# Kernel optimization log

Measured on AMD Instinct MI355X. Metric: run time of the kernel, lower is better.

The kernel has to match this reference:

```python
import jax, jax.numpy as jnp
import numpy as np

EMBED_DIM = 1024
K_DIM = 64
NUM_HEADS = 16


def setup_inputs() -> dict:
    key = jax.random.key(0)
    kx, kq, kk, kv, kw = jax.random.split(key, 5)
    x = jax.random.normal(kx, (4, 2048, EMBED_DIM), dtype=jnp.float32)
    # per-head weights stacked along a leading head axis (torch.randn init)
    wq = jax.random.normal(kq, (NUM_HEADS, EMBED_DIM, K_DIM), dtype=jnp.float32)
    wk = jax.random.normal(kk, (NUM_HEADS, EMBED_DIM, K_DIM), dtype=jnp.float32)
    wv = jax.random.normal(kv, (NUM_HEADS, EMBED_DIM, K_DIM), dtype=jnp.float32)
    w = jax.random.normal(kw, (NUM_HEADS * K_DIM, EMBED_DIM), dtype=jnp.float32)
    return {"x": x, "wq": wq, "wk": wk, "wv": wv, "w": w}


def reference(x, wq, wk, wv, w):
    # x: [B,S,D]; wq/wk/wv: [H,D,K]; w: [H*K, D]
    q = jnp.einsum('bsd,hdk->bhsk', x, wq)
    k = jnp.einsum('bsd,hdk->bhsk', x, wk)
    v = jnp.einsum('bsd,hdk->bhsk', x, wv)
    scale = 1.0 / jnp.sqrt(jnp.asarray(K_DIM, x.dtype))
    scores = jnp.einsum('bhsk,bhtk->bhst', q, k) * scale  # [B,H,S,S]
    attn = jax.nn.softmax(scores, axis=-1)
    ctx = jnp.einsum('bhst,bhtk->bhsk', attn, v)  # [B,H,S,K]
    B, H, S, K = ctx.shape
    # concat heads along last dim in head order (matches torch.cat of per-head outs)
    heads = jnp.transpose(ctx, (0, 2, 1, 3)).reshape(B, S, H * K)
    return jnp.matmul(heads, w)  # [B,S,D]
```

## Files before the change

kernel.cpp:

```cpp
#include <hip/hip_runtime.h>
#include <hip/hip_bf16.h>
#include <math.h>

#define EMBED 1024
#define KD 64
#define NH 16
#define SEQ 2048
#define BATCH 4
#define BH (BATCH * NH)
#define NTOK ((size_t)BH * SEQ * KD)

typedef float4 f4;
typedef unsigned short u16;
typedef __attribute__((ext_vector_type(8))) short v8s;
typedef __attribute__((ext_vector_type(4))) float v4f;

__device__ __forceinline__ u16 f2bf(float f) {
    unsigned u = __float_as_uint(f);
    unsigned r = (u + 0x7fffu + ((u >> 16) & 1u)) >> 16;
    return (u16)r;
}
__device__ __forceinline__ float bf2f(u16 h) {
    return __uint_as_float(((unsigned)h) << 16);
}

__device__ __forceinline__ void gload_lds16(const void* g, void* l) {
    __builtin_amdgcn_global_load_lds(
        (const __attribute__((address_space(1))) unsigned int*)g,
        (__attribute__((address_space(3))) unsigned int*)l, 16, 0, 0);
}

__global__ __launch_bounds__(256)
void convert_all_kernel(const float* __restrict__ x,
                        const float* __restrict__ wq, const float* __restrict__ wk,
                        const float* __restrict__ wv, const float* __restrict__ w,
                        u16* __restrict__ xh, u16* __restrict__ xl,
                        u16* __restrict__ Wth, u16* __restrict__ Wtl,
                        u16* __restrict__ OWth, u16* __restrict__ OWtl)
{
    int b = blockIdx.x;
    if (b < 8192) {
        size_t i = ((size_t)b * 256 + threadIdx.x) * 4;
        f4 v = *(const f4*)(x + i);
        u16 h0 = f2bf(v.x), h1 = f2bf(v.y), h2 = f2bf(v.z), h3 = f2bf(v.w);
        u16 l0 = f2bf(v.x - bf2f(h0)), l1 = f2bf(v.y - bf2f(h1));
        u16 l2 = f2bf(v.z - bf2f(h2)), l3 = f2bf(v.w - bf2f(h3));
        uint2 H, L;
        H.x = (unsigned)h0 | ((unsigned)h1 << 16);
        H.y = (unsigned)h2 | ((unsigned)h3 << 16);
        L.x = (unsigned)l0 | ((unsigned)l1 << 16);
        L.y = (unsigned)l2 | ((unsigned)l3 << 16);
        *(uint2*)(xh + i) = H;
        *(uint2*)(xl + i) = L;
    } else if (b < 8192 + 3072) {
        int n = b - 8192;
        int mat = n >> 10, nin = n & 1023, h = nin >> 6, c = nin & 63;
        const float* __restrict__ ws = (mat == 0) ? wq : (mat == 1) ? wk : wv;
        float sc = (mat == 0) ? (0.125f * 1.4426950408889634f) : 1.0f;
        for (int d = threadIdx.x; d < EMBED; d += 256) {
            float f = ws[((size_t)h * EMBED + d) * KD + c] * sc;
            u16 hi = f2bf(f);
            u16 lo = f2bf(f - bf2f(hi));
            Wth[(size_t)n * EMBED + d] = hi;
            Wtl[(size_t)n * EMBED + d] = lo;
        }
    } else {
        int n = b - 11264;
        for (int k = threadIdx.x; k < EMBED; k += 256) {
            float f = w[(size_t)k * EMBED + n];
            u16 hi = f2bf(f);
            u16 lo = f2bf(f - bf2f(hi));
            OWth[(size_t)n * EMBED + k] = hi;
            OWtl[(size_t)n * EMBED + k] = lo;
        }
    }
}

__global__ __launch_bounds__(256)
void qkv_mfma_kernel(const u16* __restrict__ xh, const u16* __restrict__ xl,
                     const u16* __restrict__ Wth, const u16* __restrict__ Wtl,
                     u16* __restrict__ Qhi, u16* __restrict__ Qlo,
                     u16* __restrict__ Khi, u16* __restrict__ Klo,
                     u16* __restrict__ Vt)
{
    __shared__ u16 sAh[128 * 64];
    __shared__ u16 sAl[128 * 64];
    __shared__ u16 sBh[128 * 64];
    __shared__ u16 sBl[128 * 64];
    const int tid = threadIdx.x;
    const int lane = tid & 63, wid = tid >> 6;
    const int lm = lane & 15, lq = lane >> 4;
    const int wm = wid & 1, wn = wid >> 1;
    const int bid = blockIdx.y * 24 + blockIdx.x;
    const int swz = (bid & 7) * 192 + (bid >> 3);
    const int m0 = (swz / 24) * 128;
    const int n0 = (swz % 24) * 128;
    const bool three = (n0 < 2048);

    v4f acc[4][4];
#pragma unroll
    for (int mt = 0; mt < 4; ++mt)
#pragma unroll
        for (int nt = 0; nt < 4; ++nt)
            acc[mt][nt] = (v4f){0.f, 0.f, 0.f, 0.f};

    const int srow = wid * 32 + (lane >> 3);
    const int sblk = (lane & 7) ^ (lane >> 3);

    for (int k0 = 0; k0 < EMBED; k0 += 64) {
        __syncthreads();
#pragma unroll
        for (int i = 0; i < 4; ++i) {
            int row = srow + i * 8;
            size_t gA = (((size_t)(m0 + row)) << 10) + k0 + sblk * 8;
            size_t gB = (((size_t)(n0 + row)) << 10) + k0 + sblk * 8;
            int lo = (wid * 32 + i * 8) * 128;
            gload_lds16((const char*)xh + gA * 2, (char*)sAh + lo);
            gload_lds16((const char*)Wth + gB * 2, (char*)sBh + lo);
            if (three) {
                gload_lds16((const char*)xl + gA * 2, (char*)sAl + lo);
                gload_lds16((const char*)Wtl + gB * 2, (char*)sBl + lo);
            }
        }
        asm volatile("s_waitcnt vmcnt(0)" ::: "memory");
        __syncthreads();

#pragma unroll
        for (int kks = 0; kks < 2; ++kks) {
            v8s ah[4], bh[4];
            const int ba = ((kks * 4 + lq) ^ (lm & 7)) * 8;
#pragma unroll
            for (int t = 0; t < 4; ++t) {
                int ra = wm * 64 + t * 16 + lm;
                int rb = wn * 64 + t * 16 + lm;
                ah[t] = *(const v8s*)&sAh[ra * 64 + ba];
                bh[t] = *(const v8s*)&sBh[rb * 64 + ba];
            }
            if (three) {
                v8s al[4], bl[4];
#pragma unroll
                for (int t = 0; t < 4; ++t) {
                    int ra = wm * 64 + t * 16 + lm;
                    int rb = wn * 64 + t * 16 + lm;
                    al[t] = *(const v8s*)&sAl[ra * 64 + ba];
                    bl[t] = *(const v8s*)&sBl[rb * 64 + ba];
                }
#pragma unroll
                for (int mt = 0; mt < 4; ++mt)
#pragma unroll
                    for (int nt = 0; nt < 4; ++nt) {
                        acc[mt][nt] = __builtin_amdgcn_mfma_f32_16x16x32_bf16(ah[mt], bh[nt], acc[mt][nt], 0, 0, 0);
                        acc[mt][nt] = __builtin_amdgcn_mfma_f32_16x16x32_bf16(ah[mt], bl[nt], acc[mt][nt], 0, 0, 0);
                        acc[mt][nt] = __builtin_amdgcn_mfma_f32_16x16x32_bf16(al[mt], bh[nt], acc[mt][nt], 0, 0, 0);
                    }
            } else {
#pragma unroll
                for (int mt = 0; mt < 4; ++mt)
#pragma unroll
                    for (int nt = 0; nt < 4; ++nt)
                        acc[mt][nt] = __builtin_amdgcn_mfma_f32_16x16x32_bf16(ah[mt], bh[nt], acc[mt][nt], 0, 0, 0);
            }
        }
    }

    const int mrow0 = m0 + wm * 64;
    const int ncol0 = n0 + wn * 64;
    if (!three) {
#pragma unroll
        for (int mt = 0; mt < 4; ++mt) {
            int sbase = mrow0 + mt * 16 + lq * 4;
            int bb = sbase >> 11, s = sbase & 2047;
#pragma unroll
            for (int nt = 0; nt < 4; ++nt) {
                int nin = (ncol0 + nt * 16 + lm) & 1023;
                int h = nin >> 6, cc = nin & 63;
                int bh_ = bb * NH + h;
                size_t a = ((size_t)bh_ * KD + cc) * SEQ
                         + (size_t)(((((s >> 3) ^ (cc & 7)) << 3)) | (s & 7));
                uint2 u;
                u.x = (unsigned)f2bf(acc[mt][nt][0]) | ((unsigned)f2bf(acc[mt][nt][1]) << 16);
                u.y = (unsigned)f2bf(acc[mt][nt][2]) | ((unsigned)f2bf(acc[mt][nt][3]) << 16);
                *(uint2*)(Vt + a) = u;
            }
        }
    } else {
        const bool isQ = (n0 < 1024);
#pragma unroll
        for (int mt = 0; mt < 4; ++mt) {
            int sbase = mrow0 + mt * 16 + lq * 4;
            int bb = sbase >> 11, sB = sbase & 2047;
#pragma unroll
            for (int nt = 0; nt < 4; ++nt) {
                int nin = (ncol0 + nt * 16 + lm) & 1023;
                int h = nin >> 6, cc = nin & 63;
                int bh_ = bb * NH + h;
#pragma unroll
                for (int r = 0; r < 4; ++r) {
                    int s = sB + r;
                    float f = acc[mt][nt][r];
                    u16 hi = f2bf(f);
                    u16 lo = f2bf(f - bf2f(hi));
                    if (isQ) {
                        size_t a = ((size_t)bh_ * SEQ + s) * KD + cc;
                        Qhi[a] = hi;
                        Qlo[a] = lo;
                    } else {
                        int ccp = ((((cc >> 3) ^ (s & 7)) << 3) | (cc & 7));
                        size_t a = ((size_t)bh_ * SEQ + s) * KD + ccp;
                        Khi[a] = hi;
                        Klo[a] = lo;
                    }
                }
            }
        }
    }
}

__global__ __launch_bounds__(512)
void attn_kernel(const u16* __restrict__ Qhi, const u16* __restrict__ Qlo,
                 const u16* __restrict__ Khi, const u16* __restrict__ Klo,
                 const u16* __restrict__ Vt,  u16* __restrict__ headsb)
{
    __shared__ u16 sKV[2][3][64 * 64];
    __shared__ u16 sPs[128 * 64];

    const int tid = threadIdx.x;
    const int lane = tid & 63, wid = tid >> 6;
    const int lm = lane & 15, lq = lane >> 4;
    const int psw = (lm & 7) << 3;
    const int rowbase = (wid >> 1) * 32 + (wid & 1) * 16;
    const int q0 = blockIdx.y * 128;
    const int bh = blockIdx.x;
    const int bb = bh >> 4, h = bh & 15;

    v8s qh[2], ql[2];
#pragma unroll
    for (int kk = 0; kk < 2; ++kk) {
        size_t g = ((size_t)bh * SEQ + q0 + rowbase + lm) * KD + kk * 32 + lq * 8;
        qh[kk] = *(const v8s*)(Qhi + g);
        ql[kk] = *(const v8s*)(Qlo + g);
    }

    v8s vones;
#pragma unroll
    for (int i = 0; i < 8; ++i) vones[i] = (short)0x3F80;
    const v4f z4 = (v4f){0.f, 0.f, 0.f, 0.f};

    int bpaddr[4];
#pragma unroll
    for (int r = 0; r < 4; ++r)
        bpaddr[r] = (((lane & 48) | (lq * 4 + r)) << 2);

    v4f ctx[4], lcol;
    float mrun = -INFINITY;
    lcol = (v4f){0.f, 0.f, 0.f, 0.f};
#pragma unroll
    for (int nt = 0; nt < 4; ++nt)
        ctx[nt] = (v4f){0.f, 0.f, 0.f, 0.f};

    const size_t kbase = (size_t)bh * SEQ * KD;
    const char* gKh = (const char*)(Khi + kbase);
    const char* gKl = (const char*)(Klo + kbase);
    const int ko = wid * 1024;
    const char* gV = (const char*)(Vt + ((size_t)bh * KD + wid * 8 + (lane >> 3)) * SEQ)
                   + (lane & 7) * 16;

    auto STAGE = [&](int t0, int buf) {
        int kb = t0 * 128 + ko + lane * 16;
        gload_lds16(gKh + kb, (char*)sKV[buf][0] + ko);
        gload_lds16(gKl + kb, (char*)sKV[buf][1] + ko);
        gload_lds16(gV + t0 * 2, (char*)sKV[buf][2] + ko);
    };

    STAGE(0, 0);

    int cur = 0;
    for (int t0 = 0; t0 < SEQ; t0 += 64, cur ^= 1) {
        asm volatile("s_waitcnt vmcnt(0)" ::: "memory");
        __syncthreads();
        if (t0 + 64 < SEQ) STAGE(t0 + 64, cur ^ 1);
        const u16* sKhi = sKV[cur][0];
        const u16* sKlo = sKV[cur][1];
        const u16* sVt  = sKV[cur][2];

        v4f sc[4];
        __builtin_amdgcn_s_setprio(1);
#pragma unroll
        for (int kt = 0; kt < 4; ++kt) {
            int key = kt * 16 + lm;
            int blk = lq ^ (key & 7);
            v8s kh16 = *(const v8s*)&sKhi[key * 64 + blk * 8];
            v8s kl16 = *(const v8s*)&sKlo[key * 64 + blk * 8];
            sc[kt] = __builtin_amdgcn_mfma_f32_16x16x32_bf16(kh16, qh[0], z4, 0, 0, 0);
            sc[kt] = __builtin_amdgcn_mfma_f32_16x16x32_bf16(kl16, qh[0], sc[kt], 0, 0, 0);
            sc[kt] = __builtin_amdgcn_mfma_f32_16x16x32_bf16(kh16, ql[0], sc[kt], 0, 0, 0);
        }
#pragma unroll
        for (int kt = 0; kt < 4; ++kt) {
            int key = kt * 16 + lm;
            int blk = (4 + lq) ^ (key & 7);
            v8s kh16 = *(const v8s*)&sKhi[key * 64 + blk * 8];
            v8s kl16 = *(const v8s*)&sKlo[key * 64 + blk * 8];
            sc[kt] = __builtin_amdgcn_mfma_f32_16x16x32_bf16(kh16, qh[1], sc[kt], 0, 0, 0);
            sc[kt] = __builtin_amdgcn_mfma_f32_16x16x32_bf16(kl16, qh[1], sc[kt], 0, 0, 0);
            sc[kt] = __builtin_amdgcn_mfma_f32_16x16x32_bf16(kh16, ql[1], sc[kt], 0, 0, 0);
        }
        __builtin_amdgcn_s_setprio(0);

        float m0v = fmaxf(fmaxf(fmaxf(sc[0][0], sc[0][1]), sc[0][2]), sc[0][3]);
        float m1v = fmaxf(fmaxf(fmaxf(sc[1][0], sc[1][1]), sc[1][2]), sc[1][3]);
        float m2v = fmaxf(fmaxf(fmaxf(sc[2][0], sc[2][1]), sc[2][2]), sc[2][3]);
        float m3v = fmaxf(fmaxf(fmaxf(sc[3][0], sc[3][1]), sc[3][2]), sc[3][3]);
        float mx = fmaxf(fmaxf(fmaxf(m0v, m1v), m2v), m3v);
        mx = fmaxf(mx, __shfl_xor(mx, 16));
        mx = fmaxf(mx, __shfl_xor(mx, 32));

        if (!__all((int)(mx <= mrun + 8.f))) {
            float mold = mrun;
            float mnew = fmaxf(mold, mx);
            float a = __builtin_amdgcn_exp2f(mold - mnew);
            mrun = mnew;
#pragma unroll
            for (int r = 0; r < 4; ++r) {
                float ar = __uint_as_float(
                    __builtin_amdgcn_ds_bpermute(bpaddr[r], __float_as_uint(a)));
                lcol[r] *= ar;
#pragma unroll
                for (int nt = 0; nt < 4; ++nt)
                    ctx[nt][r] *= ar;
            }
        }

        {
            u16* pbase = &sPs[(rowbase + lm) * 64];
#pragma unroll
            for (int kt = 0; kt < 4; ++kt) {
                unsigned u0 = __float_as_uint(__builtin_amdgcn_exp2f(sc[kt][0] - mrun));
                unsigned u1 = __float_as_uint(__builtin_amdgcn_exp2f(sc[kt][1] - mrun));
                unsigned u2 = __float_as_uint(__builtin_amdgcn_exp2f(sc[kt][2] - mrun));
                unsigned u3 = __float_as_uint(__builtin_amdgcn_exp2f(sc[kt][3] - mrun));
                uint2 pk;
                pk.x = __builtin_amdgcn_perm(u1, u0, 0x07060302);
                pk.y = __builtin_amdgcn_perm(u3, u2, 0x07060302);
                *(uint2*)&pbase[(kt * 16 + lq * 4) ^ psw] = pk;
            }
        }

        __builtin_amdgcn_s_setprio(1);
#pragma unroll
        for (int kk2 = 0; kk2 < 2; ++kk2) {
            v8s a = *(const v8s*)&sPs[(rowbase + lm) * 64 + ((kk2 * 32 + lq * 8) ^ psw)];
#pragma unroll
            for (int nt = 0; nt < 4; ++nt) {
                int hd = nt * 16 + lm;
                int blk = (kk2 * 4 + lq) ^ (hd & 7);
                v8s b = *(const v8s*)&sVt[hd * 64 + blk * 8];
                ctx[nt] = __builtin_amdgcn_mfma_f32_16x16x32_bf16(a, b, ctx[nt], 0, 0, 0);
            }
            lcol = __builtin_amdgcn_mfma_f32_16x16x32_bf16(a, vones, lcol, 0, 0, 0);
        }
        __builtin_amdgcn_s_setprio(0);
    }

#pragma unroll
    for (int r = 0; r < 4; ++r) {
        int row = q0 + rowbase + lq * 4 + r;
        float inv = 1.0f / lcol[r];
        u16* dst = headsb + ((size_t)bb * SEQ + row) * EMBED + h * KD;
#pragma unroll
        for (int nt = 0; nt < 4; ++nt)
            dst[nt * 16 + lm] = f2bf(ctx[nt][r] * inv);
    }
}

__global__ __launch_bounds__(256)
void out_mfma_kernel(const u16* __restrict__ headsb,
                     const u16* __restrict__ OWth, const u16* __restrict__ OWtl,
                     float* __restrict__ out)
{
    __shared__ u16 sA[128 * 64];
    __shared__ u16 sBh[128 * 64];
    __shared__ u16 sBl[128 * 64];
    const int tid = threadIdx.x;
    const int lane = tid & 63, wid = tid >> 6;
    const int lm = lane & 15, lq = lane >> 4;
    const int wm = wid & 1, wn = wid >> 1;
    const int bid = blockIdx.y * 8 + blockIdx.x;
    const int swz = (bid & 7) * 64 + (bid >> 3);
    const int m0 = (swz / 8) * 128;
    const int n0 = (swz % 8) * 128;

    v4f acc[4][4];
#pragma unroll
    for (int mt = 0; mt < 4; ++mt)
#pragma unroll
        for (int nt = 0; nt < 4; ++nt)
            acc[mt][nt] = (v4f){0.f, 0.f, 0.f, 0.f};

    const int srow = wid * 32 + (lane >> 3);
    const int sblk = (lane & 7) ^ (lane >> 3);

    for (int k0 = 0; k0 < EMBED; k0 += 64) {
        __syncthreads();
#pragma unroll
        for (int i = 0; i < 4; ++i) {
            int row = srow + i * 8;
            size_t gA = (((size_t)(m0 + row)) << 10) + k0 + sblk * 8;
            size_t gB = (((size_t)(n0 + row)) << 10) + k0 + sblk * 8;
            int lo = (wid * 32 + i * 8) * 128;
            gload_lds16((const char*)headsb + gA * 2, (char*)sA + lo);
            gload_lds16((const char*)OWth + gB * 2, (char*)sBh + lo);
            gload_lds16((const char*)OWtl + gB * 2, (char*)sBl + lo);
        }
        asm volatile("s_waitcnt vmcnt(0)" ::: "memory");
        __syncthreads();

#pragma unroll
        for (int kks = 0; kks < 2; ++kks) {
            const int ba = ((kks * 4 + lq) ^ (lm & 7)) * 8;
            v8s ah[4], bh[4], bl[4];
#pragma unroll
            for (int t = 0; t < 4; ++t) {
                int ra = wm * 64 + t * 16 + lm;
                int rb = wn * 64 + t * 16 + lm;
                ah[t] = *(const v8s*)&sA[ra * 64 + ba];
                bh[t] = *(const v8s*)&sBh[rb * 64 + ba];
                bl[t] = *(const v8s*)&sBl[rb * 64 + ba];
            }
#pragma unroll
            for (int mt = 0; mt < 4; ++mt)
#pragma unroll
                for (int nt = 0; nt < 4; ++nt) {
                    acc[mt][nt] = __builtin_amdgcn_mfma_f32_16x16x32_bf16(ah[mt], bh[nt], acc[mt][nt], 0, 0, 0);
                    acc[mt][nt] = __builtin_amdgcn_mfma_f32_16x16x32_bf16(ah[mt], bl[nt], acc[mt][nt], 0, 0, 0);
                }
        }
    }

    const int mrow0 = m0 + wm * 64;
    const int ncol0 = n0 + wn * 64;
#pragma unroll
    for (int mt = 0; mt < 4; ++mt) {
        int sbase = mrow0 + mt * 16 + lq * 4;
#pragma unroll
        for (int nt = 0; nt < 4; ++nt) {
            int n = ncol0 + nt * 16 + lm;
#pragma unroll
            for (int r = 0; r < 4; ++r)
                out[(size_t)(sbase + r) * EMBED + n] = acc[mt][nt][r];
        }
    }
}

extern "C" void kernel_launch(void* const* d_in, const int* in_sizes, int n_in,
                              void* d_out, int out_size, void* d_ws, size_t ws_size,
                              hipStream_t stream) {
    const float* x  = (const float*)d_in[0];
    const float* wq = (const float*)d_in[1];
    const float* wk = (const float*)d_in[2];
    const float* wv = (const float*)d_in[3];
    const float* w  = (const float*)d_in[4];
    float* out = (float*)d_out;

    u16* Qhi = (u16*)d_ws;
    u16* Qlo = Qhi + NTOK;
    u16* Khi = Qlo + NTOK;
    u16* Klo = Khi + NTOK;
    u16* Vt  = Klo + NTOK;
    u16* xh  = Vt + NTOK;
    u16* xl  = xh + NTOK;
    u16* Wth = xl + NTOK;
    u16* Wtl = Wth + (size_t)3072 * 1024;
    u16* OWth = Wtl + (size_t)3072 * 1024;
    u16* OWtl = OWth + (size_t)1024 * 1024;
    u16* headsb = xh;

    convert_all_kernel<<<12288, 256, 0, stream>>>(x, wq, wk, wv, w,
                                                  xh, xl, Wth, Wtl, OWth, OWtl);

    dim3 g1(24, 64);
    qkv_mfma_kernel<<<g1, 256, 0, stream>>>(xh, xl, Wth, Wtl, Qhi, Qlo, Khi, Klo, Vt);

    dim3 g2(BH, SEQ / 128);
    attn_kernel<<<g2, 512, 0, stream>>>(Qhi, Qlo, Khi, Klo, Vt, headsb);

    dim3 g3(8, 64);
    out_mfma_kernel<<<g3, 256, 0, stream>>>(headsb, OWth, OWtl, out);
}
```

Measured before the change: 406.6 us.

## Software-pipeline QK^T one tile ahead of softmax and PV in attention loop

Restructures the attention inner loop so the QK^T MFMAs for the next key tile are issued before the softmax and PV of the current tile. K buffers stay double-buffered and V becomes triple-buffered, with prefetch moved two tiles ahead. The loop is unrolled by two, alternating score register sets. The aim is to overlap matrix-core work with the exp/max VALU work and to hide load latency, at the cost of more registers and LDS, which could lower occupancy.

```diff
diff --git a/kernel.cpp b/kernel.cpp
--- a/kernel.cpp
+++ b/kernel.cpp
@@ -221,7 +221,8 @@
                  const u16* __restrict__ Khi, const u16* __restrict__ Klo,
                  const u16* __restrict__ Vt,  u16* __restrict__ headsb)
 {
-    __shared__ u16 sKV[2][3][64 * 64];
+    __shared__ u16 sK[2][2][64 * 64];
+    __shared__ u16 sV[3][64 * 64];
     __shared__ u16 sPs[128 * 64];
 
     const int tid = threadIdx.x;
@@ -265,25 +266,16 @@
     const char* gV = (const char*)(Vt + ((size_t)bh * KD + wid * 8 + (lane >> 3)) * SEQ)
                    + (lane & 7) * 16;
 
-    auto STAGE = [&](int t0, int buf) {
-        int kb = t0 * 128 + ko + lane * 16;
-        gload_lds16(gKh + kb, (char*)sKV[buf][0] + ko);
-        gload_lds16(gKl + kb, (char*)sKV[buf][1] + ko);
-        gload_lds16(gV + t0 * 2, (char*)sKV[buf][2] + ko);
+    auto STAGE_K = [&](int t0s, int buf) {
+        int kb = t0s * 128 + ko + lane * 16;
+        gload_lds16(gKh + kb, (char*)sK[buf][0] + ko);
+        gload_lds16(gKl + kb, (char*)sK[buf][1] + ko);
     };
-
-    STAGE(0, 0);
-
-    int cur = 0;
-    for (int t0 = 0; t0 < SEQ; t0 += 64, cur ^= 1) {
-        asm volatile("s_waitcnt vmcnt(0)" ::: "memory");
-        __syncthreads();
-        if (t0 + 64 < SEQ) STAGE(t0 + 64, cur ^ 1);
-        const u16* sKhi = sKV[cur][0];
-        const u16* sKlo = sKV[cur][1];
-        const u16* sVt  = sKV[cur][2];
-
-        v4f sc[4];
+    auto STAGE_V = [&](int t0s, int buf) {
+        gload_lds16(gV + t0s * 2, (char*)sV[buf] + ko);
+    };
+
+    auto QK = [&](const u16* sKhi, const u16* sKlo, v4f* sc) {
         __builtin_amdgcn_s_setprio(1);
 #pragma unroll
         for (int kt = 0; kt < 4; ++kt) {
@@ -306,11 +298,23 @@
             sc[kt] = __builtin_amdgcn_mfma_f32_16x16x32_bf16(kh16, ql[1], sc[kt], 0, 0, 0);
         }
         __builtin_amdgcn_s_setprio(0);
-
-        float m0v = fmaxf(fmaxf(fmaxf(sc[0][0], sc[0][1]), sc[0][2]), sc[0][3]);
-        float m1v = fmaxf(fmaxf(fmaxf(sc[1][0], sc[1][1]), sc[1][2]), sc[1][3]);
-        float m2v = fmaxf(fmaxf(fmaxf(sc[2][0], sc[2][1]), sc[2][2]), sc[2][3]);
-        float m3v = fmaxf(fmaxf(fmaxf(sc[3][0], sc[3][1]), sc[3][2]), sc[3][3]);
+    };
+
+    auto BODY = [&](int t0, int ti, v4f* scP, v4f* scN) {
+        asm volatile("s_waitcnt vmcnt(0)" ::: "memory");
+        __syncthreads();
+        const int vc  = ti % 3;
+        if (t0 + 128 < SEQ) {
+            STAGE_K(t0 + 128, ti & 1);
+            STAGE_V(t0 + 128, (ti + 2) % 3);
+        }
+        if (t0 + 64 < SEQ)
+            QK(sK[(ti + 1) & 1][0], sK[(ti + 1) & 1][1], scN);
+
+        float m0v = fmaxf(fmaxf(fmaxf(scP[0][0], scP[0][1]), scP[0][2]), scP[0][3]);
+        float m1v = fmaxf(fmaxf(fmaxf(scP[1][0], scP[1][1]), scP[1][2]), scP[1][3]);
+        float m2v = fmaxf(fmaxf(fmaxf(scP[2][0], scP[2][1]), scP[2][2]), scP[2][3]);
+        float m3v = fmaxf(fmaxf(fmaxf(scP[3][0], scP[3][1]), scP[3][2]), scP[3][3]);
         float mx = fmaxf(fmaxf(fmaxf(m0v, m1v), m2v), m3v);
         mx = fmaxf(mx, __shfl_xor(mx, 16));
         mx = fmaxf(mx, __shfl_xor(mx, 32));
@@ -335,10 +339,10 @@
             u16* pbase = &sPs[(rowbase + lm) * 64];
 #pragma unroll
             for (int kt = 0; kt < 4; ++kt) {
-                unsigned u0 = __float_as_uint(__builtin_amdgcn_exp2f(sc[kt][0] - mrun));
-                unsigned u1 = __float_as_uint(__builtin_amdgcn_exp2f(sc[kt][1] - mrun));
-                unsigned u2 = __float_as_uint(__builtin_amdgcn_exp2f(sc[kt][2] - mrun));
-                unsigned u3 = __float_as_uint(__builtin_amdgcn_exp2f(sc[kt][3] - mrun));
+                unsigned u0 = __float_as_uint(__builtin_amdgcn_exp2f(scP[kt][0] - mrun));
+                unsigned u1 = __float_as_uint(__builtin_amdgcn_exp2f(scP[kt][1] - mrun));
+                unsigned u2 = __float_as_uint(__builtin_amdgcn_exp2f(scP[kt][2] - mrun));
+                unsigned u3 = __float_as_uint(__builtin_amdgcn_exp2f(scP[kt][3] - mrun));
                 uint2 pk;
                 pk.x = __builtin_amdgcn_perm(u1, u0, 0x07060302);
                 pk.y = __builtin_amdgcn_perm(u3, u2, 0x07060302);
@@ -346,6 +350,7 @@
             }
         }
 
+        const u16* sVt = sV[vc];
         __builtin_amdgcn_s_setprio(1);
 #pragma unroll
         for (int kk2 = 0; kk2 < 2; ++kk2) {
@@ -360,6 +365,19 @@
             lcol = __builtin_amdgcn_mfma_f32_16x16x32_bf16(a, vones, lcol, 0, 0, 0);
         }
         __builtin_amdgcn_s_setprio(0);
+    };
+
+    STAGE_K(0, 0);  STAGE_V(0, 0);
+    STAGE_K(64, 1); STAGE_V(64, 1);
+    asm volatile("s_waitcnt vmcnt(0)" ::: "memory");
+    __syncthreads();
+    v4f scA[4], scB[4];
+    QK(sK[0][0], sK[0][1], scA);
+
+    for (int t0 = 0; t0 < SEQ; t0 += 128) {
+        int ti = t0 >> 6;
+        BODY(t0,      ti,     scA, scB);
+        BODY(t0 + 64, ti + 1, scB, scA);
     }
 
 #pragma unroll
```

After: 420.5 us. 1.03x slower.
